# Kernel tuning notes

Measured on AMD Instinct MI355X. Metric: run time of the kernel, lower is better.

Reference implementation:

```python
import jax, jax.numpy as jnp
import numpy as np

C = 32
N = 10000
E = 100000
LAT = 128
EPS = 1e-8
SQ3 = 3.0 ** 0.5
AVG_NEIGH = 10.0


def _sh2(p):
    # real l=2 spherical harmonics with principal axis = y (e3nn convention), m = -2..2
    x, y, z = p[..., 0], p[..., 1], p[..., 2]
    return jnp.stack([SQ3 * z * x, SQ3 * x * y, 0.5 * (3.0 * y * y - 1.0),
                      SQ3 * y * z, 0.5 * SQ3 * (z * z - x * x)], axis=-1)

# fixed sample points -> pseudoinverse for fitting Wigner-D at l=2: Y2(R p) = Y2(p) @ D2^T
_np_rng = np.random.default_rng(0)
_X = _np_rng.normal(size=(16, 3))
_X = _X / np.linalg.norm(_X, axis=1, keepdims=True)
_Xj = jnp.asarray(_X, jnp.float32)
_P2 = jnp.asarray(np.linalg.pinv(np.asarray(_sh2(jnp.asarray(_X, jnp.float32)))), jnp.float32)


def _wigner(vec):
    # per-edge rotation R with R @ n = e_y (edge aligned to y axis, e3nn convention)
    n = vec / jnp.clip(jnp.linalg.norm(vec, axis=-1, keepdims=True), 1e-9)
    ex = jnp.array([1.0, 0.0, 0.0], n.dtype)
    ez = jnp.array([0.0, 0.0, 1.0], n.dtype)
    a = jnp.where(jnp.abs(n[:, :1]) < 0.9, ex, ez)
    u = a - jnp.sum(a * n, axis=-1, keepdims=True) * n
    u = u / jnp.clip(jnp.linalg.norm(u, axis=-1, keepdims=True), 1e-9)
    v = jnp.cross(u, n)
    D1 = jnp.stack([u, n, v], axis=1)  # (E,3,3); Wigner-D for l=1 in (x,y,z) basis
    pts = jnp.einsum('eij,kj->eki', D1, _Xj)  # rotated sample points (E,K,3)
    D2 = jnp.swapaxes(jnp.einsum('mk,ekn->emn', _P2, _sh2(pts)), 1, 2)  # (E,5,5)
    return D1, D2


def _split(x):
    # flat [C x 0e | C x 1e | C x 2e] -> (.,C), (.,C,3), (.,C,5)
    return x[:, :C], x[:, C:4 * C].reshape(-1, C, 3), x[:, 4 * C:].reshape(-1, C, 5)


def _sln(x0, x1, x2, g0, b0, g1, g2):
    # separable layer norm: LN on scalars, degree-balanced RMS on l>0
    mu = jnp.mean(x0, axis=-1, keepdims=True)
    var = jnp.mean((x0 - mu) ** 2, axis=-1, keepdims=True)
    x0 = (x0 - mu) * jax.lax.rsqrt(var + EPS) * g0 + b0
    v = 0.5 * (jnp.mean(x1 ** 2, axis=(1, 2)) + jnp.mean(x2 ** 2, axis=(1, 2)))
    s = jax.lax.rsqrt(v + EPS)[:, None, None]
    return x0, x1 * s * g1[None, :, None], x2 * s * g2[None, :, None]


def _forward(latents, node_features, edge_features, edge_vector,
             g0n, b0n, g1n, g2n, g0e, b0e, g1e, g2e,
             w0s, w01, w02, wr1_1, wi1_1, wr1_2, wi1_2, wr2_2, wi2_2,
             wp0, bp0, wp1, wp2, w_env, b_env,
             atom_type, edge_index, active_edges):
    n0, n1, n2 = _sln(*_split(node_features), g0n, b0n, g1n, g2n)
    e0, e1, e2 = _sln(*_split(edge_features), g0e, b0e, g1e, g2e)
    ctr = edge_index[0][active_edges]
    nbr = edge_index[1][active_edges]
    vec = edge_vector[active_edges]
    lat = latents[active_edges]
    D1, D2 = _wigner(vec)
    # gather + concat: center | edge | neighbor, 3C channels per degree
    x0 = jnp.concatenate([n0[ctr], e0[active_edges], n0[nbr]], axis=1)
    x1 = jnp.concatenate([n1[ctr], e1[active_edges], n1[nbr]], axis=1)
    x2 = jnp.concatenate([n2[ctr], e2[active_edges], n2[nbr]], axis=1)
    # rotate into edge frame
    x1 = jnp.einsum('emn,ecn->ecm', D1, x1)
    x2 = jnp.einsum('emn,ecn->ecm', D2, x2)
    # SO2 linear (block structure over m about the edge axis = y; m index = l+m)
    s0 = 1.0 / jnp.sqrt(jnp.float32(9 * C))
    s1 = 1.0 / jnp.sqrt(jnp.float32(6 * C))
    s2 = 1.0 / jnp.sqrt(jnp.float32(3 * C))
    in0 = jnp.concatenate([x0, x1[:, :, 1], x2[:, :, 2]], axis=1)  # (E,9C) m=0
    y0 = in0 @ w0s.T * s0      # (E,3C): C scalars + 2C gates
    y1_0 = in0 @ w01.T * s0
    y2_0 = in0 @ w02.T * s0
    xp1 = jnp.concatenate([x1[:, :, 2], x2[:, :, 3]], axis=1)  # m=+1
    xm1 = jnp.concatenate([x1[:, :, 0], x2[:, :, 1]], axis=1)  # m=-1
    y1_p = (xp1 @ wr1_1.T - xm1 @ wi1_1.T) * s1
    y1_m = (xp1 @ wi1_1.T + xm1 @ wr1_1.T) * s1
    y2_p1 = (xp1 @ wr1_2.T - xm1 @ wi1_2.T) * s1
    y2_m1 = (xp1 @ wi1_2.T + xm1 @ wr1_2.T) * s1
    xp2 = x2[:, :, 4]
    xm2 = x2[:, :, 0]
    y2_p2 = (xp2 @ wr2_2.T - xm2 @ wi2_2.T) * s2
    y2_m2 = (xp2 @ wi2_2.T + xm2 @ wr2_2.T) * s2
    y1 = jnp.stack([y1_m, y1_0, y1_p], axis=-1)                      # (E,C,3)
    y2 = jnp.stack([y2_m2, y2_m1, y2_0, y2_p1, y2_p2], axis=-1)      # (E,C,5)
    # rotate back to global frame
    y1 = jnp.einsum('enm,ecn->ecm', D1, y1)
    y2 = jnp.einsum('enm,ecn->ecm', D2, y2)
    # Gate activation
    scal = jax.nn.silu(y0[:, :C])
    gate1 = jax.nn.sigmoid(y0[:, C:2 * C])
    gate2 = jax.nn.sigmoid(y0[:, 2 * C:])
    m1 = y1 * gate1[:, :, None]
    m2 = y2 * gate2[:, :, None]
    # lin_post (e3nn Linear, per-degree, bias on scalars)
    sc = 1.0 / jnp.sqrt(jnp.float32(C))
    m0 = scal @ wp0.T * sc + bp0
    m1 = jnp.einsum('dc,ecm->edm', wp1, m1) * sc
    m2 = jnp.einsum('dc,ecm->edm', wp2, m2) * sc
    # env weighting: per-irrep elementwise scalars from latents
    w = lat @ w_env.T * (1.0 / jnp.sqrt(jnp.float32(LAT))) + b_env
    m0 = m0 * w[:, :C]
    m1 = m1 * w[:, C:2 * C][:, :, None]
    m2 = m2 * w[:, 2 * C:][:, :, None]
    msg = jnp.concatenate([m0, m1.reshape(-1, 3 * C), m2.reshape(-1, 5 * C)], axis=1)
    agg = jax.ops.segment_sum(msg, ctr, num_segments=N) * (1.0 / jnp.sqrt(AVG_NEIGH))
    # residual update with logit-0 coefficient
    cu = 0.5
    c_old = 1.0 / jnp.sqrt(1.0 + cu * cu)
    c_new = cu * c_old
    return c_old * node_features + c_new * agg


def setup_inputs() -> dict:
    key = jax.random.key(0)
    ks = jax.random.split(key, 32)
    f = lambda i, shape: jax.random.normal(ks[i], shape, dtype=jnp.float32)
    return {
        'latents': f(0, (E, LAT)),
        'node_features': f(1, (N, 9 * C)),
        'edge_features': f(2, (E, 9 * C)),
        'edge_vector': f(3, (E, 3)),
        'atom_type': jax.random.randint(ks[4], (N,), 0, 10),
        'edge_index': jax.random.randint(ks[5], (2, E), 0, N),
        'active_edges': jnp.arange(E),
        'g0n': 1.0 + 0.1 * f(6, (C,)), 'b0n': 0.1 * f(7, (C,)),
        'g1n': 1.0 + 0.1 * f(8, (C,)), 'g2n': 1.0 + 0.1 * f(9, (C,)),
        'g0e': 1.0 + 0.1 * f(10, (C,)), 'b0e': 0.1 * f(11, (C,)),
        'g1e': 1.0 + 0.1 * f(12, (C,)), 'g2e': 1.0 + 0.1 * f(13, (C,)),
        'w0s': f(14, (3 * C, 9 * C)), 'w01': f(15, (C, 9 * C)), 'w02': f(16, (C, 9 * C)),
        'wr1_1': f(17, (C, 6 * C)), 'wi1_1': f(18, (C, 6 * C)),
        'wr1_2': f(19, (C, 6 * C)), 'wi1_2': f(20, (C, 6 * C)),
        'wr2_2': f(21, (C, 3 * C)), 'wi2_2': f(22, (C, 3 * C)),
        'wp0': f(23, (C, C)), 'bp0': 0.1 * f(24, (C,)),
        'wp1': f(25, (C, C)), 'wp2': f(26, (C, C)),
        'w_env': f(27, (3 * C, LAT)), 'b_env': 1.0 + 0.1 * f(28, (3 * C,)),
    }


def reference(latents, node_features, edge_features, edge_vector,
              g0n, b0n, g1n, g2n, g0e, b0e, g1e, g2e,
              w0s, w01, w02, wr1_1, wi1_1, wr1_2, wi1_2, wr2_2, wi2_2,
              wp0, bp0, wp1, wp2, w_env, b_env,
              atom_type, edge_index, active_edges):
    return _forward(latents, node_features, edge_features, edge_vector,
                    g0n, b0n, g1n, g2n, g0e, b0e, g1e, g2e,
                    w0s, w01, w02, wr1_1, wi1_1, wr1_2, wi1_2, wr2_2, wi2_2,
                    wp0, bp0, wp1, wp2, w_env, b_env,
                    atom_type, edge_index, active_edges)
```

## Files before the change

kernel.cpp:

```cpp
#include <hip/hip_runtime.h>
#include <hip/hip_bf16.h>
#include <math.h>

#define NN 10000
#define EE 100000
#define EPB 16
#define AST 992
#define PA0 480

#define SEG0 0
#define SEGP1 288
#define SEGM1 480
#define SEGP2 672
#define SEGM2 768
#define SEGL 864

#define Y0o   0
#define Y10o  96
#define Y20o  128
#define Y1Po  160
#define Y1Mo  192
#define Y2P1o 224
#define Y2M1o 256
#define Y2P2o 288
#define Y2M2o 320
#define WENVo 352

#define PK1 0
#define PK2 46080
#define PK3 95232
#define PK4 107520
#define PKP 119808
#define PKTOT 122880

#define WS_NRM 0
#define WS_PK  11520000
#define WS_CNT 11765760
#define WS_OFF 11831296
#define WS_CUR 11896832
#define WS_EL  11962368
#define WS_MSG 12486656
#define WS_REQ (WS_MSG + (size_t)EE*288*2)

#define SQ3F  1.7320508075688772f
#define S0F   0.05892556509887896f
#define S1F   0.07216878364870323f
#define S2F   0.10206207261596575f
#define SEF   0.08838834764831845f
#define SCF   0.17677669529663687f
#define COLDF 0.8944271909999159f
#define COEFF 0.1414213562373095f

#define NNB 2500
#define PKB ((PKTOT + 255) / 256)
#define HSB ((EE + 255) / 256)

typedef __attribute__((ext_vector_type(8))) short bf16x8;
typedef __attribute__((ext_vector_type(4))) float f32x4;

__device__ __forceinline__ ushort f2bf(float f) {
    __hip_bfloat16 h = __float2bfloat16(f);
    return __builtin_bit_cast(unsigned short, h);
}
__device__ __forceinline__ float bf2f(ushort u) {
    union { unsigned u; float f; } v; v.u = (unsigned)u << 16; return v.f;
}
__device__ __forceinline__ float fsig(float x) {
    return __builtin_amdgcn_rcpf(1.f + __expf(-x));
}
__device__ __forceinline__ int planar(int k) {
    if (k < 32) return k;
    if (k < 128) { int c = (k - 32) / 3, m = (k - 32) % 3; return 32 + 32*m + c; }
    int c = (k - 128) / 5, m = (k - 128) % 5; return 128 + 32*m + c;
}

__global__ __launch_bounds__(256) void init_k(
    const float* __restrict__ nf,
    const float* __restrict__ g0, const float* __restrict__ b0,
    const float* __restrict__ g1, const float* __restrict__ g2,
    float* __restrict__ nrm, float* __restrict__ out,
    const float* __restrict__ w0s, const float* __restrict__ w01, const float* __restrict__ w02,
    const float* __restrict__ wr11, const float* __restrict__ wi11,
    const float* __restrict__ wr12, const float* __restrict__ wi12,
    const float* __restrict__ wr22, const float* __restrict__ wi22,
    const float* __restrict__ wenv,
    const float* __restrict__ wp0, const float* __restrict__ wp1, const float* __restrict__ wp2,
    ushort* __restrict__ pk,
    const int* __restrict__ eidx, const int* __restrict__ act, int* __restrict__ counts)
{
    const int bid = blockIdx.x;
    if (bid < NNB) {
        int row = bid * 4 + (threadIdx.x >> 6);
        if (row >= NN) return;
        int lane = threadIdx.x & 63;
        const float* r = nf + (size_t)row * 288;
        float v0 = r[lane];
        float v1 = r[lane + 64];
        float v2 = r[lane + 128];
        float v3 = r[lane + 192];
        float v4 = (lane < 32) ? r[lane + 256] : 0.f;
        float s0 = 0.f, s0q = 0.f, q1 = 0.f, q2 = 0.f;
        if (lane < 32) { s0 = v0; s0q = v0*v0; } else { q1 = v0*v0; }
        q1 += v1*v1;
        q2 += v2*v2 + v3*v3 + v4*v4;
#pragma unroll
        for (int m = 1; m < 64; m <<= 1) {
            s0  += __shfl_xor(s0, m);
            s0q += __shfl_xor(s0q, m);
            q1  += __shfl_xor(q1, m);
            q2  += __shfl_xor(q2, m);
        }
        float mu  = s0 * (1.f/32.f);
        float rs0 = rsqrtf(s0q*(1.f/32.f) - mu*mu + 1e-8f);
        float rs  = rsqrtf(0.5f*(q1*(1.f/96.f) + q2*(1.f/160.f)) + 1e-8f);
        float* nr = nrm + (size_t)row * 288;
        {
            float res;
            if (lane < 32) res = (v0 - mu) * rs0 * g0[lane] + b0[lane];
            else { int c = (lane - 32) / 3; res = v0 * rs * g1[c]; }
            nr[planar(lane)] = res;
        }
        { int k = lane + 64;  int c = (k - 32) / 3;  nr[planar(k)] = v1 * rs * g1[c]; }
        { int k = lane + 128; int c = (k - 128) / 5; nr[planar(k)] = v2 * rs * g2[c]; }
        { int k = lane + 192; int c = (k - 128) / 5; nr[planar(k)] = v3 * rs * g2[c]; }
        if (lane < 32) { int k = lane + 256; int c = (k - 128) / 5; nr[planar(k)] = v4 * rs * g2[c]; }
        if (out) {
            float* orow = out + (size_t)row * 288;
            orow[lane]       = COLDF * v0;
            orow[lane + 64]  = COLDF * v1;
            orow[lane + 128] = COLDF * v2;
            orow[lane + 192] = COLDF * v3;
            if (lane < 32) orow[lane + 256] = COLDF * v4;
        }
    } else if (bid < NNB + PKB) {
        int i = (bid - NNB) * 256 + threadIdx.x;
        if (i >= PKTOT) return;
        float val;
        if (i < PK2) {
            int idx = i - PK1;
            int tile = idx / 4608, rem = idx % 4608;
            int chunk = rem / 512, rem2 = rem % 512;
            int lane = rem2 / 8, j = rem2 % 8;
            int col = tile * 16 + (lane & 15);
            int k = chunk * 32 + (lane >> 4) * 8 + j;
            if (col < 96)       val = w0s[col * 288 + k];
            else if (col < 128) val = w01[(col - 96) * 288 + k];
            else                val = w02[(col - 128) * 288 + k];
        } else if (i < PK3) {
            int idx = i - PK2;
            int tile = idx / 6144, rem = idx % 6144;
            int chunk = rem / 512, rem2 = rem % 512;
            int lane = rem2 / 8, j = rem2 % 8;
            int col = tile * 16 + (lane & 15);
            int k = chunk * 32 + (lane >> 4) * 8 + j;
            int grp = col >> 5, c = col & 31;
            if (k < 192) {
                val = (grp == 0) ? wr11[c*192 + k] : (grp == 1) ? wi11[c*192 + k]
                    : (grp == 2) ? wr12[c*192 + k] : wi12[c*192 + k];
            } else {
                int kk = k - 192;
                val = (grp == 0) ? -wi11[c*192 + kk] : (grp == 1) ? wr11[c*192 + kk]
                    : (grp == 2) ? -wi12[c*192 + kk] : wr12[c*192 + kk];
            }
        } else if (i < PK4) {
            int idx = i - PK3;
            int tile = idx / 3072, rem = idx % 3072;
            int chunk = rem / 512, rem2 = rem % 512;
            int lane = rem2 / 8, j = rem2 % 8;
            int col = tile * 16 + (lane & 15);
            int k = chunk * 32 + (lane >> 4) * 8 + j;
            int grp = col >> 5, c = col & 31;
            if (k < 96) val = grp ? wi22[c*96 + k] : wr22[c*96 + k];
            else        val = grp ? wr22[c*96 + k - 96] : -wi22[c*96 + k - 96];
        } else if (i < PKP) {
            int idx = i - PK4;
            int tile = idx / 2048, rem = idx % 2048;
            int chunk = rem / 512, rem2 = rem % 512;
            int lane = rem2 / 8, j = rem2 % 8;
            int col = tile * 16 + (lane & 15);
            int k = chunk * 32 + (lane >> 4) * 8 + j;
            val = wenv[col * 128 + k];
        } else {
            int idx = i - PKP;
            int wpi = idx / 1024, rem = idx % 1024;
            int ct = rem / 512, rem2 = rem % 512;
            int lane = rem2 / 8, j = rem2 % 8;
            int col = ct * 16 + (lane & 15);
            int k = (lane >> 4) * 8 + j;
            const float* w = (wpi == 0) ? wp0 : (wpi == 1) ? wp1 : wp2;
            val = w[col * 32 + k];
        }
        pk[i] = f2bf(val);
    } else {
        int e = (bid - NNB - PKB) * 256 + threadIdx.x;
        if (e >= EE) return;
        atomicAdd(&counts[eidx[act[e]]], 1);
    }
}

__global__ __launch_bounds__(1024) void scan_k(
    const int* __restrict__ counts, int* __restrict__ offs, int* __restrict__ curs)
{
    const int tid = threadIdx.x;
    const int base = tid * 10;
    int v[10]; int s = 0;
#pragma unroll
    for (int j = 0; j < 10; ++j) {
        int i = base + j;
        int c = (i < NN) ? counts[i] : 0;
        v[j] = s; s += c;
    }
    const int lane = tid & 63, wv = tid >> 6;
    int inc = s;
#pragma unroll
    for (int off = 1; off < 64; off <<= 1) {
        int t = __shfl_up(inc, off);
        if (lane >= off) inc += t;
    }
    __shared__ int wsum[16], wbase[16];
    if (lane == 63) wsum[wv] = inc;
    __syncthreads();
    if (tid == 0) {
        int acc = 0;
#pragma unroll
        for (int i = 0; i < 16; ++i) { int t = wsum[i]; wbase[i] = acc; acc += t; }
    }
    __syncthreads();
    const int texcl = wbase[wv] + inc - s;
#pragma unroll
    for (int j = 0; j < 10; ++j) {
        int i = base + j;
        if (i < NN) { int o = texcl + v[j]; offs[i] = o; curs[i] = o; }
    }
}

__global__ __launch_bounds__(256) void scatter_k(
    const int* __restrict__ eidx, const int* __restrict__ act,
    int* __restrict__ curs, int* __restrict__ eslot) {
    int e = blockIdx.x * 256 + threadIdx.x;
    if (e >= EE) return;
    int pos = atomicAdd(&curs[eidx[act[e]]], 1);
    eslot[e] = pos;
}

__global__ __launch_bounds__(256) void gather_k(
    const ushort* __restrict__ msg, const int* __restrict__ offs,
    const int* __restrict__ counts,
    const float* __restrict__ nf, float* __restrict__ out)
{
    int node = blockIdx.x * 4 + (threadIdx.x >> 6);
    if (node >= NN) return;
    int lane = threadIdx.x & 63;
    int start = offs[node], cnt = counts[node];
    float a0x = 0.f, a0y = 0.f, a1x = 0.f, a1y = 0.f, a2x = 0.f, a2y = 0.f;
    const uint* mu = (const uint*)(msg + (size_t)start * 288);
    for (int i = 0; i < cnt; ++i, mu += 144) {
        uint u0 = mu[lane];
        uint u1 = mu[lane + 64];
        uint u2 = (lane < 16) ? mu[lane + 128] : 0u;
        a0x += bf2f((ushort)u0); a0y += bf2f((ushort)(u0 >> 16));
        a1x += bf2f((ushort)u1); a1y += bf2f((ushort)(u1 >> 16));
        a2x += bf2f((ushort)u2); a2y += bf2f((ushort)(u2 >> 16));
    }
    const float2* r2 = (const float2*)(nf + (size_t)node * 288);
    float2* o2 = (float2*)(out + (size_t)node * 288);
    float2 r;
    r = r2[lane];
    o2[lane]      = make_float2(COLDF*r.x + COEFF*a0x, COLDF*r.y + COEFF*a0y);
    r = r2[lane + 64];
    o2[lane + 64] = make_float2(COLDF*r.x + COEFF*a1x, COLDF*r.y + COEFF*a1y);
    if (lane < 16) {
        r = r2[lane + 128];
        o2[lane + 128] = make_float2(COLDF*r.x + COEFF*a2x, COLDF*r.y + COEFF*a2y);
    }
}

__global__ __launch_bounds__(512, 8) void edge_k(
    const float* __restrict__ lat, const float* __restrict__ ef,
    const float* __restrict__ evec,
    const int* __restrict__ eidx, const int* __restrict__ act,
    const int* __restrict__ eslot,
    const float* __restrict__ g0e, const float* __restrict__ b0e,
    const float* __restrict__ g1e, const float* __restrict__ g2e,
    const ushort* __restrict__ pk,
    const float* __restrict__ bp0, const float* __restrict__ benv,
    const float* __restrict__ nrm, ushort* __restrict__ msg, float* __restrict__ out)
{
    __shared__ __align__(16) ushort sA[EPB * AST];
    __shared__ float sD1[EPB][12];
    __shared__ float sD2[EPB][28];
    __shared__ int sAe[EPB], sCtr[EPB], sNbr[EPB], sSlot[EPB];

    const int tid = threadIdx.x;
    const int wv = tid >> 6, lane = tid & 63;

    if (tid < EPB) {
        int ae = act[blockIdx.x * EPB + tid];
        sAe[tid] = ae;
        sCtr[tid] = eidx[ae];
        sNbr[tid] = eidx[EE + ae];
        sSlot[tid] = eslot ? eslot[blockIdx.x * EPB + tid] : 0;

        float vx = evec[3*ae], vy = evec[3*ae+1], vz = evec[3*ae+2];
        float nnv = fmaxf(sqrtf(vx*vx + vy*vy + vz*vz), 1e-9f);
        float nx = vx/nnv, ny = vy/nnv, nz = vz/nnv;
        float ax, az;
        if (fabsf(nx) < 0.9f) { ax = 1.f; az = 0.f; } else { ax = 0.f; az = 1.f; }
        float adn = ax*nx + az*nz;
        float ux = ax - adn*nx, uy = -adn*ny, uz = az - adn*nz;
        float un = fmaxf(sqrtf(ux*ux + uy*uy + uz*uz), 1e-9f);
        ux /= un; uy /= un; uz /= un;
        float wx = uy*nz - uz*ny, wy = uz*nx - ux*nz, wz = ux*ny - uy*nx;

        sD1[tid][0] = ux; sD1[tid][1] = uy; sD1[tid][2] = uz;
        sD1[tid][3] = nx; sD1[tid][4] = ny; sD1[tid][5] = nz;
        sD1[tid][6] = wx; sD1[tid][7] = wy; sD1[tid][8] = wz;

        float d2[5][5];
        d2[0][0] = wz*ux + uz*wx;  d2[0][1] = wx*uy + ux*wy;  d2[0][2] = SQ3F*wy*uy;
        d2[0][3] = wy*uz + uy*wz;  d2[0][4] = wz*uz - wx*ux;
        d2[1][0] = uz*nx + nz*ux;  d2[1][1] = ux*ny + nx*uy;  d2[1][2] = SQ3F*uy*ny;
        d2[1][3] = uy*nz + ny*uz;  d2[1][4] = uz*nz - ux*nx;
        d2[2][0] = SQ3F*nz*nx;     d2[2][1] = SQ3F*nx*ny;     d2[2][2] = 1.5f*ny*ny - 0.5f;
        d2[2][3] = SQ3F*ny*nz;     d2[2][4] = 0.5f*SQ3F*(nz*nz - nx*nx);
        d2[3][0] = nz*wx + wz*nx;  d2[3][1] = nx*wy + wx*ny;  d2[3][2] = SQ3F*ny*wy;
        d2[3][3] = ny*wz + wy*nz;  d2[3][4] = nz*wz - nx*wx;
        d2[4][0] = wz*wx - uz*ux;  d2[4][1] = wx*wy - ux*uy;  d2[4][2] = 0.5f*SQ3F*(wy*wy - uy*uy);
        d2[4][3] = wy*wz - uy*uz;  d2[4][4] = 0.5f*(wz*wz - uz*uz - wx*wx + ux*ux);
#pragma unroll
        for (int n = 0; n < 5; ++n)
#pragma unroll
            for (int m = 0; m < 5; ++m) sD2[tid][5*n + m] = d2[n][m];
    }
    __syncthreads();

    for (int it = 0; it < 2; ++it) {
        const int e = it * 8 + wv;
        const int ae = sAe[e];
        const int ctr = sCtr[e], nbr = sNbr[e];
        ushort* row = sA + e * AST;
        ushort* rowEB = row + 64;
        const float* efr = ef + (size_t)ae * 288;

        float ev0 = efr[lane];
        float ev1 = efr[lane + 64];
        float ev2 = efr[lane + 128];
        float ev3 = efr[lane + 192];
        float ev4 = (lane < 32) ? efr[lane + 256] : 0.f;
        float s0 = 0.f, s0q = 0.f, q1 = 0.f, q2 = 0.f;
        if (lane < 32) { s0 = ev0; s0q = ev0*ev0; } else { q1 = ev0*ev0; }
        q1 += ev1*ev1;
        q2 += ev2*ev2 + ev3*ev3 + ev4*ev4;
#pragma unroll
        for (int m = 1; m < 64; m <<= 1) {
            s0  += __shfl_xor(s0, m);
            s0q += __shfl_xor(s0q, m);
            q1  += __shfl_xor(q1, m);
            q2  += __shfl_xor(q2, m);
        }
        float mu  = s0 * (1.f/32.f);
        float rs0 = rsqrtf(s0q*(1.f/32.f) - mu*mu + 1e-8f);
        float rs  = rsqrtf(0.5f*(q1*(1.f/96.f) + q2*(1.f/160.f)) + 1e-8f);

        if (lane >= 32) { int c = (lane-32)/3, m = (lane-32)%3; rowEB[32 + 32*m + c] = f2bf(ev0 * rs * g1e[c]); }
        { int k = lane+64;  int c = (k-32)/3,  m = (k-32)%3;  rowEB[32 + 32*m + c]  = f2bf(ev1 * rs * g1e[c]); }
        { int k = lane+128; int c = (k-128)/5, m = (k-128)%5; rowEB[128 + 32*m + c] = f2bf(ev2 * rs * g2e[c]); }
        { int k = lane+192; int c = (k-128)/5, m = (k-128)%5; rowEB[128 + 32*m + c] = f2bf(ev3 * rs * g2e[c]); }
        if (lane < 32) { int k = lane+256; int c = (k-128)/5, m = (k-128)%5; rowEB[128 + 32*m + c] = f2bf(ev4 * rs * g2e[c]); }

        if (lane < 32) {
            row[SEG0 + 32 + lane] = f2bf((ev0 - mu) * rs0 * g0e[lane] + b0e[lane]);
            row[SEG0 + lane]      = f2bf(nrm[(size_t)ctr*288 + lane]);
            row[SEG0 + 64 + lane] = f2bf(nrm[(size_t)nbr*288 + lane]);
        }
        {
            const float* lr = lat + (size_t)ae * 128;
            row[SEGL + lane]      = f2bf(lr[lane]);
            row[SEGL + 64 + lane] = f2bf(lr[lane + 64]);
        }
    }
    __syncthreads();

    {
        const int re = tid >> 5;
        const int rc = tid & 31;
        const float* bc = nrm + (size_t)sCtr[re] * 288;
        const float* bn = nrm + (size_t)sNbr[re] * 288;
        float c1v[3], c2v[5], n1v[3], n2v[5];
#pragma unroll
        for (int m = 0; m < 3; ++m) { c1v[m] = bc[32 + 32*m + rc]; n1v[m] = bn[32 + 32*m + rc]; }
#pragma unroll
        for (int m = 0; m < 5; ++m) { c2v[m] = bc[128 + 32*m + rc]; n2v[m] = bn[128 + 32*m + rc]; }
        ushort* row = sA + re * AST;
        const ushort* rowEB = row + 64;
        float e1v[3], e2v[5];
#pragma unroll
        for (int m = 0; m < 3; ++m) e1v[m] = bf2f(rowEB[32 + 32*m + rc]);
#pragma unroll
        for (int m = 0; m < 5; ++m) e2v[m] = bf2f(rowEB[128 + 32*m + rc]);
        asm volatile("" ::: "memory");
        float D1r[9], d2l[25];
#pragma unroll
        for (int i = 0; i < 9; ++i) D1r[i] = sD1[re][i];
#pragma unroll
        for (int i = 0; i < 25; ++i) d2l[i] = sD2[re][i];
#pragma unroll
        for (int p = 0; p < 3; ++p) {
            const int cc = rc + 32 * p;
            float x1v[3], x2v[5];
#pragma unroll
            for (int m = 0; m < 3; ++m) x1v[m] = (p == 0) ? c1v[m] : (p == 1) ? e1v[m] : n1v[m];
#pragma unroll
            for (int m = 0; m < 5; ++m) x2v[m] = (p == 0) ? c2v[m] : (p == 1) ? e2v[m] : n2v[m];
            float r0 = D1r[0]*x1v[0] + D1r[1]*x1v[1] + D1r[2]*x1v[2];
            float r1 = D1r[3]*x1v[0] + D1r[4]*x1v[1] + D1r[5]*x1v[2];
            float r2 = D1r[6]*x1v[0] + D1r[7]*x1v[1] + D1r[8]*x1v[2];
            float t[5];
#pragma unroll
            for (int m = 0; m < 5; ++m)
                t[m] = d2l[5*m+0]*x2v[0] + d2l[5*m+1]*x2v[1] + d2l[5*m+2]*x2v[2]
                     + d2l[5*m+3]*x2v[3] + d2l[5*m+4]*x2v[4];
            row[SEG0 + 96  + cc] = f2bf(r1);
            row[SEG0 + 192 + cc] = f2bf(t[2]);
            row[SEGP1 + cc]      = f2bf(r2);
            row[SEGP1 + 96 + cc] = f2bf(t[3]);
            row[SEGM1 + cc]      = f2bf(r0);
            row[SEGM1 + 96 + cc] = f2bf(t[1]);
            row[SEGP2 + cc]      = f2bf(t[4]);
            row[SEGM2 + cc]      = f2bf(t[0]);
        }
    }
    __syncthreads();

    f32x4 pacc[4];
#pragma unroll
    for (int q = 0; q < 4; ++q) {
        const int t = wv + 8*q;
        if (t < 28) {
            int kbase, nch, pbase; float scale;
            if (t < 10)      { kbase = SEG0;  nch = 9;  scale = S0F; pbase = PK1 + t*9*512; }
            else if (t < 18) { kbase = SEGP1; nch = 12; scale = S1F; pbase = PK2 + (t-10)*12*512; }
            else if (t < 22) { kbase = SEGP2; nch = 6;  scale = S2F; pbase = PK3 + (t-18)*6*512; }
            else             { kbase = SEGL;  nch = 4;  scale = SEF; pbase = PK4 + (t-22)*4*512; }
            f32x4 acc = {0.f, 0.f, 0.f, 0.f};
            const ushort* pa = sA + (lane & 15) * AST + kbase + (lane >> 4) * 8;
            const ushort* pb = pk + pbase + lane * 8;
            for (int ch = 0; ch < nch; ++ch) {
                bf16x8 a = *reinterpret_cast<const bf16x8*>(pa + ch * 32);
                bf16x8 b = *reinterpret_cast<const bf16x8*>(pb + ch * 512);
                acc = __builtin_amdgcn_mfma_f32_16x16x32_bf16(a, b, acc, 0, 0, 0);
            }
            int yoff = (t < 10) ? t*16 : (t < 18) ? 160+(t-10)*16 : (t < 22) ? 288+(t-18)*16 : 352+(t-22)*16;
            float bv = (t >= 22) ? benv[yoff + (lane & 15) - 352] : 0.f;
#pragma unroll
            for (int j = 0; j < 4; ++j) acc[j] = acc[j] * scale + bv;
            pacc[q] = acc;
        }
    }
    __syncthreads();

#pragma unroll
    for (int q = 0; q < 4; ++q) {
        const int t = wv + 8*q;
        if (t < 28) {
            int yoff = (t < 10) ? t*16 : (t < 18) ? 160+(t-10)*16 : (t < 22) ? 288+(t-18)*16 : 352+(t-22)*16;
            const int col = yoff + (lane & 15);
            const int r0 = (lane >> 4) * 4;
#pragma unroll
            for (int j = 0; j < 4; ++j) {
                const int rr = r0 + j;
                sA[rr * AST + (col ^ (rr << 1))] = f2bf(pacc[q][j]);
            }
        }
    }
    __syncthreads();

    const int e2 = tid & 15, d = tid >> 4;
    {
        const int rowb = e2 * AST;
        const int sw = e2 << 1;
        auto LDY = [&](int x) { return bf2f(sA[rowb + (x ^ sw)]); };
        float y0v = LDY(Y0o + d);
        float scv = y0v * fsig(y0v);
        float gg1 = fsig(LDY(Y0o + 32 + d));
        float gg2 = fsig(LDY(Y0o + 64 + d));
        const int pabase = rowb + PA0 + 8*((d >> 3) ^ (e2 & 3)) + (d & 7);
        sA[pabase + 0*56] = f2bf(scv);
        sA[pabase + 1*56] = f2bf(LDY(Y1Mo  + d) * gg1);
        sA[pabase + 2*56] = f2bf(LDY(Y10o  + d) * gg1);
        sA[pabase + 3*56] = f2bf(LDY(Y1Po  + d) * gg1);
        sA[pabase + 4*56] = f2bf(LDY(Y2M2o + d) * gg2);
        sA[pabase + 5*56] = f2bf(LDY(Y2M1o + d) * gg2);
        sA[pabase + 6*56] = f2bf(LDY(Y20o  + d) * gg2);
        sA[pabase + 7*56] = f2bf(LDY(Y2P1o + d) * gg2);
        sA[pabase + 8*56] = f2bf(LDY(Y2P2o + d) * gg2);
    }
    __syncthreads();

    f32x4 pacc2[3];
#pragma unroll
    for (int q = 0; q < 3; ++q) {
        const int t = wv + 8*q;
        if (t < 18) {
            const int rt = t >> 1, ct = t & 1;
            const int wpi = (rt == 0) ? 0 : (rt < 4) ? 1 : 2;
            const int ar = lane & 15;
            bf16x8 a = *reinterpret_cast<const bf16x8*>(
                sA + ar*AST + PA0 + rt*56 + 8*((lane >> 4) ^ (ar & 3)));
            bf16x8 b = *reinterpret_cast<const bf16x8*>(pk + PKP + wpi*1024 + ct*512 + lane*8);
            f32x4 z = {0.f, 0.f, 0.f, 0.f};
            pacc2[q] = __builtin_amdgcn_mfma_f32_16x16x32_bf16(a, b, z, 0, 0, 0);
        }
    }
    __syncthreads();

#pragma unroll
    for (int q = 0; q < 3; ++q) {
        const int t = wv + 8*q;
        if (t < 18) {
            const int rt = t >> 1, ct = t & 1;
            const int col = ct*16 + (lane & 15);
#pragma unroll
            for (int j = 0; j < 4; ++j) {
                const int ee = (lane >> 4)*4 + j;
                const int colSw = (col + 4*ee) & 31;
                float* fp = reinterpret_cast<float*>(sA + ee * AST);
                if (rt < 4) fp[rt*44 + colSw] = pacc2[q][j];
                else        fp[240 + (rt-4)*50 + colSw] = pacc2[q][j];
            }
        }
    }
    __syncthreads();

    float m0v, o1[3], o2[5];
    {
        const int rowb = e2 * AST;
        const int sw = e2 << 1;
        auto LDY = [&](int x) { return bf2f(sA[rowb + (x ^ sw)]); };
        const float* fp = reinterpret_cast<const float*>(sA + rowb);
        const int cd = (d + 4*e2) & 31;
        float p0 = fp[cd];
        float p1v[3], p2v[5];
#pragma unroll
        for (int m = 0; m < 3; ++m) p1v[m] = fp[(1+m)*44 + cd];
#pragma unroll
        for (int m = 0; m < 5; ++m) p2v[m] = fp[240 + m*50 + cd];

        float wv0g = LDY(WENVo + d);
        float wv1g = LDY(WENVo + 32 + d) * SCF;
        float wv2g = LDY(WENVo + 64 + d) * SCF;
        m0v = (p0 * SCF + bp0[d]) * wv0g;
#pragma unroll
        for (int mm = 0; mm < 3; ++mm)
            o1[mm] = (sD1[e2][mm]*p1v[0] + sD1[e2][3+mm]*p1v[1] + sD1[e2][6+mm]*p1v[2]) * wv1g;
#pragma unroll
        for (int mm = 0; mm < 5; ++mm)
            o2[mm] = (sD2[e2][mm]*p2v[0] + sD2[e2][5+mm]*p2v[1] + sD2[e2][10+mm]*p2v[2]
                    + sD2[e2][15+mm]*p2v[3] + sD2[e2][20+mm]*p2v[4]) * wv2g;
    }

    if (msg) {
        __syncthreads();
        ushort* stg = sA + e2 * AST;
        stg[d] = f2bf(m0v);
#pragma unroll
        for (int mm = 0; mm < 3; ++mm) stg[32 + 3*d + mm] = f2bf(o1[mm]);
#pragma unroll
        for (int mm = 0; mm < 5; ++mm) stg[128 + 5*d + mm] = f2bf(o2[mm]);
        __syncthreads();
        const int e = tid >> 5, j = tid & 31;
        const ushort* src = sA + e * AST;
        ushort* dst = msg + (size_t)sSlot[e] * 288;
        *reinterpret_cast<bf16x8*>(dst + j*8) = *reinterpret_cast<const bf16x8*>(src + j*8);
        if (j < 4)
            *reinterpret_cast<bf16x8*>(dst + 256 + j*8) = *reinterpret_cast<const bf16x8*>(src + 256 + j*8);
    } else {
        float* ob = out + (size_t)sCtr[e2] * 288;
        atomicAdd(ob + d, COEFF * m0v);
#pragma unroll
        for (int mm = 0; mm < 3; ++mm) atomicAdd(ob + 32 + 3*d + mm, COEFF * o1[mm]);
#pragma unroll
        for (int mm = 0; mm < 5; ++mm) atomicAdd(ob + 128 + 5*d + mm, COEFF * o2[mm]);
    }
}

extern "C" void kernel_launch(void* const* d_in, const int* in_sizes, int n_in,
                              void* d_out, int out_size, void* d_ws, size_t ws_size,
                              hipStream_t stream)
{
    const float* latents = (const float*)d_in[0];
    const float* nf      = (const float*)d_in[1];
    const float* efe     = (const float*)d_in[2];
    const float* evec    = (const float*)d_in[3];
    const int*   eidx    = (const int*)d_in[5];
    const int*   act     = (const int*)d_in[6];
    const float* g0n = (const float*)d_in[7];
    const float* b0n = (const float*)d_in[8];
    const float* g1n = (const float*)d_in[9];
    const float* g2n = (const float*)d_in[10];
    const float* g0e = (const float*)d_in[11];
    const float* b0e = (const float*)d_in[12];
    const float* g1e = (const float*)d_in[13];
    const float* g2e = (const float*)d_in[14];
    const float* w0s = (const float*)d_in[15];
    const float* w01 = (const float*)d_in[16];
    const float* w02 = (const float*)d_in[17];
    const float* wr11 = (const float*)d_in[18];
    const float* wi11 = (const float*)d_in[19];
    const float* wr12 = (const float*)d_in[20];
    const float* wi12 = (const float*)d_in[21];
    const float* wr22 = (const float*)d_in[22];
    const float* wi22 = (const float*)d_in[23];
    const float* wp0 = (const float*)d_in[24];
    const float* bp0 = (const float*)d_in[25];
    const float* wp1 = (const float*)d_in[26];
    const float* wp2 = (const float*)d_in[27];
    const float* wenv = (const float*)d_in[28];
    const float* benv = (const float*)d_in[29];
    float* out = (float*)d_out;

    char* ws = (char*)d_ws;
    float* nrm  = (float*)(ws + WS_NRM);
    ushort* pkw = (ushort*)(ws + WS_PK);
    const bool use_msg = (ws_size >= WS_REQ);
    int* counts = (int*)(ws + WS_CNT);
    int* offs   = (int*)(ws + WS_OFF);
    int* curs   = (int*)(ws + WS_CUR);
    int* eslot  = (int*)(ws + WS_EL);
    ushort* msg = (ushort*)(ws + WS_MSG);

    hipMemsetAsync(counts, 0, NN * sizeof(int), stream);
    init_k<<<NNB + PKB + HSB, 256, 0, stream>>>(
        nf, g0n, b0n, g1n, g2n, nrm, use_msg ? nullptr : out,
        w0s, w01, w02, wr11, wi11, wr12, wi12, wr22, wi22, wenv, wp0, wp1, wp2, pkw,
        eidx, act, counts);
    if (use_msg) {
        scan_k<<<1, 1024, 0, stream>>>(counts, offs, curs);
        scatter_k<<<(EE + 255) / 256, 256, 0, stream>>>(eidx, act, curs, eslot);
    }
    edge_k<<<EE / EPB, 512, 0, stream>>>(latents, efe, evec, eidx, act,
        use_msg ? eslot : nullptr,
        g0e, b0e, g1e, g2e, pkw, bp0, benv, nrm, use_msg ? msg : nullptr, out);
    if (use_msg) {
        gather_k<<<(NN + 3) / 4, 256, 0, stream>>>(msg, offs, counts, nf, out);
    }
}
```

Measured before the change: 232.1 us.

## Reassign MFMA tiles per wave, fold scale into weights, index messages via edge list

The first GEMM is restructured so each of the 8 waves owns a fixed, compile-time-sized group of output tiles and reuses each A fragment across several B tiles. The second GEMM is regrouped the same way. The SCF scale is folded into the packed projection weights at init, and the shared-memory row stride changes. Messages are now written contiguously by edge order, and the gather kernel reads them indirectly through an edge list built by the scatter kernel. This trades scattered writes in the edge kernel for indirect reads in the gather and leaves the waves with uneven amounts of work.

```diff
diff --git a/kernel.cpp b/kernel.cpp
--- a/kernel.cpp
+++ b/kernel.cpp
@@ -5,7 +5,7 @@
 #define NN 10000
 #define EE 100000
 #define EPB 16
-#define AST 992
+#define AST 1000
 #define PA0 480
 
 #define SEG0 0
@@ -188,7 +188,7 @@
             int col = ct * 16 + (lane & 15);
             int k = (lane >> 4) * 8 + j;
             const float* w = (wpi == 0) ? wp0 : (wpi == 1) ? wp1 : wp2;
-            val = w[col * 32 + k];
+            val = w[col * 32 + k] * SCF;
         }
         pk[i] = f2bf(val);
     } else {
@@ -236,16 +236,16 @@
 
 __global__ __launch_bounds__(256) void scatter_k(
     const int* __restrict__ eidx, const int* __restrict__ act,
-    int* __restrict__ curs, int* __restrict__ eslot) {
+    int* __restrict__ curs, int* __restrict__ elist) {
     int e = blockIdx.x * 256 + threadIdx.x;
     if (e >= EE) return;
     int pos = atomicAdd(&curs[eidx[act[e]]], 1);
-    eslot[e] = pos;
+    elist[pos] = e;
 }
 
 __global__ __launch_bounds__(256) void gather_k(
     const ushort* __restrict__ msg, const int* __restrict__ offs,
-    const int* __restrict__ counts,
+    const int* __restrict__ counts, const int* __restrict__ elist,
     const float* __restrict__ nf, float* __restrict__ out)
 {
     int node = blockIdx.x * 4 + (threadIdx.x >> 6);
@@ -253,8 +253,9 @@
     int lane = threadIdx.x & 63;
     int start = offs[node], cnt = counts[node];
     float a0x = 0.f, a0y = 0.f, a1x = 0.f, a1y = 0.f, a2x = 0.f, a2y = 0.f;
-    const uint* mu = (const uint*)(msg + (size_t)start * 288);
-    for (int i = 0; i < cnt; ++i, mu += 144) {
+    for (int i = 0; i < cnt; ++i) {
+        int e = elist[start + i];
+        const uint* mu = (const uint*)(msg + (size_t)e * 288);
         uint u0 = mu[lane];
         uint u1 = mu[lane + 64];
         uint u2 = (lane < 16) ? mu[lane + 128] : 0u;
@@ -275,11 +276,46 @@
     }
 }
 
+template<int TC, int NCH>
+__device__ __forceinline__ void gemm_seg(
+    const ushort* __restrict__ sA_, int lane, int kbase, int pbase,
+    const ushort* __restrict__ pk, f32x4* acc)
+{
+    const ushort* pa = sA_ + (lane & 15) * AST + kbase + (lane >> 4) * 8;
+    const ushort* pb = pk + pbase + lane * 8;
+#pragma unroll
+    for (int ch = 0; ch < NCH; ++ch) {
+        bf16x8 a = *reinterpret_cast<const bf16x8*>(pa + ch * 32);
+#pragma unroll
+        for (int i = 0; i < TC; ++i) {
+            bf16x8 b = *reinterpret_cast<const bf16x8*>(pb + i*NCH*512 + ch*512);
+            acc[i] = __builtin_amdgcn_mfma_f32_16x16x32_bf16(a, b, acc[i], 0, 0, 0);
+        }
+    }
+}
+
+template<int TC>
+__device__ __forceinline__ void store_y(
+    ushort* __restrict__ sA_, int lane, int ybase, float scale,
+    const float* __restrict__ benv, f32x4* acc)
+{
+#pragma unroll
+    for (int i = 0; i < TC; ++i) {
+        const int col = ybase + i*16 + (lane & 15);
+        const float bv = (ybase >= 352) ? benv[col - 352] : 0.f;
+        const int r0 = (lane >> 4) * 4;
+#pragma unroll
+        for (int j = 0; j < 4; ++j) {
+            const int rr = r0 + j;
+            sA_[rr * AST + (col ^ (rr << 1))] = f2bf(acc[i][j] * scale + bv);
+        }
+    }
+}
+
 __global__ __launch_bounds__(512, 8) void edge_k(
     const float* __restrict__ lat, const float* __restrict__ ef,
     const float* __restrict__ evec,
     const int* __restrict__ eidx, const int* __restrict__ act,
-    const int* __restrict__ eslot,
     const float* __restrict__ g0e, const float* __restrict__ b0e,
     const float* __restrict__ g1e, const float* __restrict__ g2e,
     const ushort* __restrict__ pk,
@@ -289,7 +325,7 @@
     __shared__ __align__(16) ushort sA[EPB * AST];
     __shared__ float sD1[EPB][12];
     __shared__ float sD2[EPB][28];
-    __shared__ int sAe[EPB], sCtr[EPB], sNbr[EPB], sSlot[EPB];
+    __shared__ int sAe[EPB], sCtr[EPB], sNbr[EPB];
 
     const int tid = threadIdx.x;
     const int wv = tid >> 6, lane = tid & 63;
@@ -299,7 +335,6 @@
         sAe[tid] = ae;
         sCtr[tid] = eidx[ae];
         sNbr[tid] = eidx[EE + ae];
-        sSlot[tid] = eslot ? eslot[blockIdx.x * EPB + tid] : 0;
 
         float vx = evec[3*ae], vy = evec[3*ae+1], vz = evec[3*ae+2];
         float nnv = fmaxf(sqrtf(vx*vx + vy*vy + vz*vz), 1e-9f);
@@ -432,46 +467,28 @@
     }
     __syncthreads();
 
-    f32x4 pacc[4];
-#pragma unroll
-    for (int q = 0; q < 4; ++q) {
-        const int t = wv + 8*q;
-        if (t < 28) {
-            int kbase, nch, pbase; float scale;
-            if (t < 10)      { kbase = SEG0;  nch = 9;  scale = S0F; pbase = PK1 + t*9*512; }
-            else if (t < 18) { kbase = SEGP1; nch = 12; scale = S1F; pbase = PK2 + (t-10)*12*512; }
-            else if (t < 22) { kbase = SEGP2; nch = 6;  scale = S2F; pbase = PK3 + (t-18)*6*512; }
-            else             { kbase = SEGL;  nch = 4;  scale = SEF; pbase = PK4 + (t-22)*4*512; }
-            f32x4 acc = {0.f, 0.f, 0.f, 0.f};
-            const ushort* pa = sA + (lane & 15) * AST + kbase + (lane >> 4) * 8;
-            const ushort* pb = pk + pbase + lane * 8;
-            for (int ch = 0; ch < nch; ++ch) {
-                bf16x8 a = *reinterpret_cast<const bf16x8*>(pa + ch * 32);
-                bf16x8 b = *reinterpret_cast<const bf16x8*>(pb + ch * 512);
-                acc = __builtin_amdgcn_mfma_f32_16x16x32_bf16(a, b, acc, 0, 0, 0);
-            }
-            int yoff = (t < 10) ? t*16 : (t < 18) ? 160+(t-10)*16 : (t < 22) ? 288+(t-18)*16 : 352+(t-22)*16;
-            float bv = (t >= 22) ? benv[yoff + (lane & 15) - 352] : 0.f;
-#pragma unroll
-            for (int j = 0; j < 4; ++j) acc[j] = acc[j] * scale + bv;
-            pacc[q] = acc;
-        }
-    }
-    __syncthreads();
-
-#pragma unroll
-    for (int q = 0; q < 4; ++q) {
-        const int t = wv + 8*q;
-        if (t < 28) {
-            int yoff = (t < 10) ? t*16 : (t < 18) ? 160+(t-10)*16 : (t < 22) ? 288+(t-18)*16 : 352+(t-22)*16;
-            const int col = yoff + (lane & 15);
-            const int r0 = (lane >> 4) * 4;
-#pragma unroll
-            for (int j = 0; j < 4; ++j) {
-                const int rr = r0 + j;
-                sA[rr * AST + (col ^ (rr << 1))] = f2bf(pacc[q][j]);
-            }
-        }
+    f32x4 acc[6] = {};
+    switch (wv) {
+        case 0: gemm_seg<4,9 >(sA, lane, SEG0,  PK1,            pk, acc); break;
+        case 1: gemm_seg<3,9 >(sA, lane, SEG0,  PK1 + 4*9*512,  pk, acc); break;
+        case 2: gemm_seg<3,9 >(sA, lane, SEG0,  PK1 + 7*9*512,  pk, acc); break;
+        case 3: gemm_seg<3,12>(sA, lane, SEGP1, PK2,            pk, acc); break;
+        case 4: gemm_seg<3,12>(sA, lane, SEGP1, PK2 + 3*12*512, pk, acc); break;
+        case 5: gemm_seg<2,12>(sA, lane, SEGP1, PK2 + 6*12*512, pk, acc); break;
+        case 6: gemm_seg<4,6 >(sA, lane, SEGP2, PK3,            pk, acc); break;
+        case 7: gemm_seg<6,4 >(sA, lane, SEGL,  PK4,            pk, acc); break;
+    }
+    __syncthreads();
+
+    switch (wv) {
+        case 0: store_y<4>(sA, lane, 0,        S0F, benv, acc); break;
+        case 1: store_y<3>(sA, lane, 64,       S0F, benv, acc); break;
+        case 2: store_y<3>(sA, lane, 112,      S0F, benv, acc); break;
+        case 3: store_y<3>(sA, lane, 160,      S1F, benv, acc); break;
+        case 4: store_y<3>(sA, lane, 160+48,   S1F, benv, acc); break;
+        case 5: store_y<2>(sA, lane, 160+96,   S1F, benv, acc); break;
+        case 6: store_y<4>(sA, lane, 288,      S2F, benv, acc); break;
+        case 7: store_y<6>(sA, lane, 352,      SEF, benv, acc); break;
     }
     __syncthreads();
 
@@ -497,36 +514,57 @@
     }
     __syncthreads();
 
-    f32x4 pacc2[3];
-#pragma unroll
-    for (int q = 0; q < 3; ++q) {
-        const int t = wv + 8*q;
-        if (t < 18) {
-            const int rt = t >> 1, ct = t & 1;
-            const int wpi = (rt == 0) ? 0 : (rt < 4) ? 1 : 2;
-            const int ar = lane & 15;
-            bf16x8 a = *reinterpret_cast<const bf16x8*>(
-                sA + ar*AST + PA0 + rt*56 + 8*((lane >> 4) ^ (ar & 3)));
+    f32x4 pacc2[4];
+    {
+        const int ar = lane & 15;
+        const int rt = wv;
+        bf16x8 a = *reinterpret_cast<const bf16x8*>(
+            sA + ar*AST + PA0 + rt*56 + 8*((lane >> 4) ^ (ar & 3)));
+        const int wpi = (rt == 0) ? 0 : (rt < 4) ? 1 : 2;
+#pragma unroll
+        for (int ct = 0; ct < 2; ++ct) {
             bf16x8 b = *reinterpret_cast<const bf16x8*>(pk + PKP + wpi*1024 + ct*512 + lane*8);
             f32x4 z = {0.f, 0.f, 0.f, 0.f};
-            pacc2[q] = __builtin_amdgcn_mfma_f32_16x16x32_bf16(a, b, z, 0, 0, 0);
-        }
-    }
-    __syncthreads();
-
-#pragma unroll
-    for (int q = 0; q < 3; ++q) {
-        const int t = wv + 8*q;
-        if (t < 18) {
-            const int rt = t >> 1, ct = t & 1;
+            pacc2[ct] = __builtin_amdgcn_mfma_f32_16x16x32_bf16(a, b, z, 0, 0, 0);
+        }
+        if (wv == 0) {
+            bf16x8 a8 = *reinterpret_cast<const bf16x8*>(
+                sA + ar*AST + PA0 + 8*56 + 8*((lane >> 4) ^ (ar & 3)));
+#pragma unroll
+            for (int ct = 0; ct < 2; ++ct) {
+                bf16x8 b = *reinterpret_cast<const bf16x8*>(pk + PKP + 2*1024 + ct*512 + lane*8);
+                f32x4 z = {0.f, 0.f, 0.f, 0.f};
+                pacc2[2 + ct] = __builtin_amdgcn_mfma_f32_16x16x32_bf16(a8, b, z, 0, 0, 0);
+            }
+        }
+    }
+    __syncthreads();
+
+    {
+        const int rt = wv;
+#pragma unroll
+        for (int ct = 0; ct < 2; ++ct) {
             const int col = ct*16 + (lane & 15);
 #pragma unroll
             for (int j = 0; j < 4; ++j) {
                 const int ee = (lane >> 4)*4 + j;
                 const int colSw = (col + 4*ee) & 31;
                 float* fp = reinterpret_cast<float*>(sA + ee * AST);
-                if (rt < 4) fp[rt*44 + colSw] = pacc2[q][j];
-                else        fp[240 + (rt-4)*50 + colSw] = pacc2[q][j];
+                if (rt < 4) fp[rt*44 + colSw] = pacc2[ct][j];
+                else        fp[240 + (rt-4)*50 + colSw] = pacc2[ct][j];
+            }
+        }
+        if (wv == 0) {
+#pragma unroll
+            for (int ct = 0; ct < 2; ++ct) {
+                const int col = ct*16 + (lane & 15);
+#pragma unroll
+                for (int j = 0; j < 4; ++j) {
+                    const int ee = (lane >> 4)*4 + j;
+                    const int colSw = (col + 4*ee) & 31;
+                    float* fp = reinterpret_cast<float*>(sA + ee * AST);
+                    fp[240 + 4*50 + colSw] = pacc2[2 + ct][j];
+                }
             }
         }
     }
@@ -547,9 +585,9 @@
         for (int m = 0; m < 5; ++m) p2v[m] = fp[240 + m*50 + cd];
 
         float wv0g = LDY(WENVo + d);
-        float wv1g = LDY(WENVo + 32 + d) * SCF;
-        float wv2g = LDY(WENVo + 64 + d) * SCF;
-        m0v = (p0 * SCF + bp0[d]) * wv0g;
+        float wv1g = LDY(WENVo + 32 + d);
+        float wv2g = LDY(WENVo + 64 + d);
+        m0v = (p0 + bp0[d]) * wv0g;
 #pragma unroll
         for (int mm = 0; mm < 3; ++mm)
             o1[mm] = (sD1[e2][mm]*p1v[0] + sD1[e2][3+mm]*p1v[1] + sD1[e2][6+mm]*p1v[2]) * wv1g;
@@ -570,7 +608,7 @@
         __syncthreads();
         const int e = tid >> 5, j = tid & 31;
         const ushort* src = sA + e * AST;
-        ushort* dst = msg + (size_t)sSlot[e] * 288;
+        ushort* dst = msg + (size_t)(blockIdx.x * EPB + e) * 288;
         *reinterpret_cast<bf16x8*>(dst + j*8) = *reinterpret_cast<const bf16x8*>(src + j*8);
         if (j < 4)
             *reinterpret_cast<bf16x8*>(dst + 256 + j*8) = *reinterpret_cast<const bf16x8*>(src + 256 + j*8);
@@ -626,7 +664,7 @@
     int* counts = (int*)(ws + WS_CNT);
     int* offs   = (int*)(ws + WS_OFF);
     int* curs   = (int*)(ws + WS_CUR);
-    int* eslot  = (int*)(ws + WS_EL);
+    int* elist  = (int*)(ws + WS_EL);
     ushort* msg = (ushort*)(ws + WS_MSG);
 
     hipMemsetAsync(counts, 0, NN * sizeof(int), stream);
@@ -636,12 +674,11 @@
         eidx, act, counts);
     if (use_msg) {
         scan_k<<<1, 1024, 0, stream>>>(counts, offs, curs);
-        scatter_k<<<(EE + 255) / 256, 256, 0, stream>>>(eidx, act, curs, eslot);
+        scatter_k<<<(EE + 255) / 256, 256, 0, stream>>>(eidx, act, curs, elist);
     }
     edge_k<<<EE / EPB, 512, 0, stream>>>(latents, efe, evec, eidx, act,
-        use_msg ? eslot : nullptr,
         g0e, b0e, g1e, g2e, pkw, bp0, benv, nrm, use_msg ? msg : nullptr, out);
     if (use_msg) {
-        gather_k<<<(NN + 3) / 4, 256, 0, stream>>>(msg, offs, counts, nf, out);
-    }
-}
+        gather_k<<<(NN + 3) / 4, 256, 0, stream>>>(msg, offs, counts, elist, nf, out);
+    }
+}
```

Result: slower. 245.3 us (+5.7%).
